# Kernel optimization log

Measured on AMD Instinct MI355X. Metric: run time of the kernel, lower is better.

Reference implementation:

```python
import jax, jax.numpy as jnp
import numpy as np
import math


def setup_inputs() -> dict:
    key = jax.random.key(0)
    k1, k2, k3 = jax.random.split(key, 3)
    B, L, H, E = 2, 2048, 8, 64
    queries = jax.random.normal(k1, (B, L, H, E), dtype=jnp.float32)
    keys = jax.random.normal(k2, (B, L, H, E), dtype=jnp.float32)
    values = jax.random.normal(k3, (B, L, H, E), dtype=jnp.float32)
    return {"queries": queries, "keys": keys, "values": values}


def reference(queries, keys, values):
    B, L, H, E = queries.shape
    scale = 1.0 / math.sqrt(E)
    # [B,H,L,S] attention scores
    scores = jnp.einsum('blhe,bshe->bhls', queries, keys)
    # causal mask: positions s > l masked to -inf (scale * -inf stays -inf)
    causal = jnp.triu(jnp.ones((L, L), dtype=bool), k=1)  # True above diagonal
    scores = jnp.where(causal[None, None, :, :], -jnp.inf, scores)
    attn = scale * scores
    SA = jax.nn.softmax(attn, axis=-1)  # dropout p=0.0 -> identity
    V = jnp.einsum('bhls,bshd->blhd', SA, values)
    return (V, SA)
```

## Files before the change

### kernel.cpp

```cpp
#include <hip/hip_runtime.h>
#include <math.h>

#define L_DIM 2048
#define H_DIM 8
#define ROWSTRIDE 512
#define NT 512
#define QSCALE 0.18033688011112042f
#define FLT_BIG 3.402823466e+38f

typedef __attribute__((ext_vector_type(8))) short short8;
typedef __attribute__((ext_vector_type(4))) float floatx4;

__device__ __forceinline__ float fexp2(float x) {
#if __has_builtin(__builtin_amdgcn_exp2f)
    return __builtin_amdgcn_exp2f(x);
#else
    return exp2f(x);
#endif
}

__device__ __forceinline__ float flog2(float x) {
#if __has_builtin(__builtin_amdgcn_logf)
    return __builtin_amdgcn_logf(x);
#else
    return log2f(x);
#endif
}

__device__ __forceinline__ unsigned int cvtpk(float lo, float hi) {
    unsigned int r;
    asm("v_cvt_pk_bf16_f32 %0, %1, %2" : "=v"(r) : "v"(lo), "v"(hi));
    return r;
}

__device__ __forceinline__ short8 pack8(float4 a, float4 b) {
    union { unsigned int u[4]; short8 v; } pk;
    pk.u[0] = cvtpk(a.x, a.y); pk.u[1] = cvtpk(a.z, a.w);
    pk.u[2] = cvtpk(b.x, b.y); pk.u[3] = cvtpk(b.z, b.w);
    return pk.v;
}

__device__ __forceinline__ short8 pack8q(float4 a, float4 b) {
    union { unsigned int u[4]; short8 v; } pk;
    pk.u[0] = cvtpk(a.x * QSCALE, a.y * QSCALE);
    pk.u[1] = cvtpk(a.z * QSCALE, a.w * QSCALE);
    pk.u[2] = cvtpk(b.x * QSCALE, b.y * QSCALE);
    pk.u[3] = cvtpk(b.z * QSCALE, b.w * QSCALE);
    return pk.v;
}

__device__ __forceinline__ int swz(int row, int col) {
    return (row << 6) + ((((col >> 3) ^ (row & 7)) << 3) | (col & 7));
}

__global__ __launch_bounds__(NT, 4)
void attn_mfma5(const float* __restrict__ Q, const float* __restrict__ K,
                const float* __restrict__ Vv, float* __restrict__ outV,
                float* __restrict__ outSA)
{
    __shared__ __align__(16) unsigned char smem[41984];
    unsigned short* Ks = (unsigned short*)(smem);
    unsigned short* Vt = (unsigned short*)(smem + 16384);
    unsigned short* Ps = (unsigned short*)(smem + 32768);
    float* Ml = (float*)(smem + 40960);
    float* Ll = (float*)(smem + 41472);
    float* Ob = (float*)(smem);

    const int t    = threadIdx.x;
    const int lane = t & 63;
    const int w    = t >> 6;
    const int g    = w >> 2;
    const int wg   = w & 3;
    const int l15  = lane & 15;
    const int quad = lane >> 4;
    const int gc   = g << 5;

    const int bid = blockIdx.x;
    const int c   = bid & 255;
    const int hf  = bid >> 8;
    const int bh  = c & 15;
    const int p   = c >> 4;
    const int qt  = hf ? p : (31 - p);
    const int h   = bh & 7;
    const int b   = bh >> 3;
    const int q0  = qt << 6;
    const int ntiles = qt + 1;

    const float* Qb = Q  + (size_t)b * L_DIM * ROWSTRIDE + h * 64;
    const float* Kb = K  + (size_t)b * L_DIM * ROWSTRIDE + h * 64;
    const float* Vb = Vv + (size_t)b * L_DIM * ROWSTRIDE + h * 64;
    float* saBase = outSA + (size_t)(b * H_DIM + h) * L_DIM * L_DIM;

    const int sr = t >> 3, sc = (t & 7) << 3;
    const int kswz = swz(sr, sc);

    short8 aQ0, aQ1;
    {
        const float* qsrc = Qb + (size_t)(q0 + 16 * wg + l15) * ROWSTRIDE + quad * 8;
        aQ0 = pack8q(*(const float4*)(qsrc),      *(const float4*)(qsrc + 4));
        aQ1 = pack8q(*(const float4*)(qsrc + 32), *(const float4*)(qsrc + 36));
    }

    float m_r[4], l_r[4];
#pragma unroll
    for (int r = 0; r < 4; ++r) { m_r[r] = -FLT_BIG; l_r[r] = 0.f; }

    {
        const float* src = Kb + (size_t)sr * ROWSTRIDE + sc;
        *(short8*)&Ks[kswz] = pack8(*(const float4*)src, *(const float4*)(src + 4));
    }
    __syncthreads();

    for (int st = 0; st < ntiles; ++st) {
        const int cur = st & 1;
        const int stp = (st + 1 < ntiles) ? (st + 1) : st;
        const float* ksrc = Kb + (size_t)((stp << 6) + sr) * ROWSTRIDE + sc;
        float4 kf0 = *(const float4*)(ksrc);
        float4 kf1 = *(const float4*)(ksrc + 4);

        const unsigned short* Kc = Ks + (cur << 12);
        floatx4 d[2];
#pragma unroll
        for (int jj = 0; jj < 2; ++jj) {
            const int sb = gc + (jj << 4) + l15;
            short8 b0 = *(const short8*)&Kc[swz(sb, quad * 8)];
            short8 b1 = *(const short8*)&Kc[swz(sb, 32 + quad * 8)];
            floatx4 acc = {0.f, 0.f, 0.f, 0.f};
            acc = __builtin_amdgcn_mfma_f32_16x16x32_bf16(aQ0, b0, acc, 0, 0, 0);
            acc = __builtin_amdgcn_mfma_f32_16x16x32_bf16(aQ1, b1, acc, 0, 0, 0);
            d[jj] = acc;
        }
        if (st == qt) {
            const int s0 = st << 6;
#pragma unroll
            for (int r = 0; r < 4; ++r) {
                const int lrow = q0 + 16 * wg + quad * 4 + r;
                float v0 = (s0 + gc +  0 + l15 <= lrow) ? d[0][r] : -INFINITY;
                float v1 = (s0 + gc + 16 + l15 <= lrow) ? d[1][r] : -INFINITY;
                const float mnew = fmaxf(m_r[r], fmaxf(v0, v1));
                float es = fexp2(v0 - mnew) + fexp2(v1 - mnew);
                l_r[r] = l_r[r] * fexp2(m_r[r] - mnew) + es;
                m_r[r] = mnew;
            }
        } else {
#pragma unroll
            for (int r = 0; r < 4; ++r) {
                float v0 = d[0][r], v1 = d[1][r];
                const float mnew = fmaxf(m_r[r], fmaxf(v0, v1));
                float es = fexp2(v0 - mnew) + fexp2(v1 - mnew);
                l_r[r] = l_r[r] * fexp2(m_r[r] - mnew) + es;
                m_r[r] = mnew;
            }
        }
        if (st + 1 < ntiles)
            *(short8*)&Ks[((cur ^ 1) << 12) + kswz] = pack8(kf0, kf1);
        __syncthreads();
    }

#pragma unroll
    for (int r = 0; r < 4; ++r) {
#pragma unroll
        for (int mk = 1; mk < 16; mk <<= 1) {
            float mo = __shfl_xor(m_r[r], mk);
            float lo = __shfl_xor(l_r[r], mk);
            float mn = fmaxf(m_r[r], mo);
            l_r[r] = l_r[r] * fexp2(m_r[r] - mn) + lo * fexp2(mo - mn);
            m_r[r] = mn;
        }
    }

    if (l15 == 0) {
#pragma unroll
        for (int r = 0; r < 4; ++r) {
            const int row = 16 * wg + quad * 4 + r;
            Ml[g * 64 + row] = m_r[r];
            Ll[g * 64 + row] = l_r[r];
        }
    }
    {
        const float* src = Kb + (size_t)sr * ROWSTRIDE + sc;
        *(short8*)&Ks[kswz] = pack8(*(const float4*)src, *(const float4*)(src + 4));
        const float* vsrc = Vb + (size_t)sr * ROWSTRIDE + sc;
        float4 f0 = *(const float4*)(vsrc);
        float4 f1 = *(const float4*)(vsrc + 4);
        unsigned int w01 = cvtpk(f0.x, f0.y), w23 = cvtpk(f0.z, f0.w);
        unsigned int w45 = cvtpk(f1.x, f1.y), w67 = cvtpk(f1.z, f1.w);
        Vt[swz(sc + 0, sr)] = (unsigned short)w01;
        Vt[swz(sc + 1, sr)] = (unsigned short)(w01 >> 16);
        Vt[swz(sc + 2, sr)] = (unsigned short)w23;
        Vt[swz(sc + 3, sr)] = (unsigned short)(w23 >> 16);
        Vt[swz(sc + 4, sr)] = (unsigned short)w45;
        Vt[swz(sc + 5, sr)] = (unsigned short)(w45 >> 16);
        Vt[swz(sc + 6, sr)] = (unsigned short)w67;
        Vt[swz(sc + 7, sr)] = (unsigned short)(w67 >> 16);
    }
    __syncthreads();

    float c_r[4];
#pragma unroll
    for (int r = 0; r < 4; ++r) {
        const int row = 16 * wg + quad * 4 + r;
        float m0 = Ml[row], m1 = Ml[64 + row];
        float l0 = Ll[row], l1 = Ll[64 + row];
        float mf = fmaxf(m0, m1);
        float lf = l0 * fexp2(m0 - mf) + l1 * fexp2(m1 - mf);
        c_r[r] = mf + flog2(lf);
    }

    floatx4 oacc[4];
#pragma unroll
    for (int j = 0; j < 4; ++j) oacc[j] = (floatx4){0.f, 0.f, 0.f, 0.f};

    for (int st = 0; st < ntiles; ++st) {
        const int cur = st & 1;
        const int stp = (st + 1 < ntiles) ? (st + 1) : st;
        const float* ksrc = Kb + (size_t)((stp << 6) + sr) * ROWSTRIDE + sc;
        const float* vsrc = Vb + (size_t)((stp << 6) + sr) * ROWSTRIDE + sc;
        float4 kf0 = *(const float4*)(ksrc);
        float4 kf1 = *(const float4*)(ksrc + 4);
        float4 vf0 = *(const float4*)(vsrc);
        float4 vf1 = *(const float4*)(vsrc + 4);

        const unsigned short* Kc = Ks + (cur << 12);
        floatx4 d[2];
#pragma unroll
        for (int jj = 0; jj < 2; ++jj) {
            const int sb = gc + (jj << 4) + l15;
            short8 b0 = *(const short8*)&Kc[swz(sb, quad * 8)];
            short8 b1 = *(const short8*)&Kc[swz(sb, 32 + quad * 8)];
            floatx4 acc = {0.f, 0.f, 0.f, 0.f};
            acc = __builtin_amdgcn_mfma_f32_16x16x32_bf16(aQ0, b0, acc, 0, 0, 0);
            acc = __builtin_amdgcn_mfma_f32_16x16x32_bf16(aQ1, b1, acc, 0, 0, 0);
            d[jj] = acc;
        }
        const int s0 = st << 6;
        if (st == qt) {
#pragma unroll
            for (int r = 0; r < 4; ++r) {
                const int lrow = q0 + 16 * wg + quad * 4 + r;
                float* sap = saBase + (size_t)lrow * L_DIM + s0 + gc + l15;
                const float cr = c_r[r];
                float p0 = (s0 + gc +      l15 <= lrow) ? fexp2(d[0][r] - cr) : 0.0f;
                float p1 = (s0 + gc + 16 + l15 <= lrow) ? fexp2(d[1][r] - cr) : 0.0f;
                sap[0] = p0; sap[16] = p1;
                unsigned int pw = cvtpk(p0, p1);
                const int prow = 16 * wg + quad * 4 + r;
                Ps[swz(prow, gc + l15)]      = (unsigned short)pw;
                Ps[swz(prow, gc + 16 + l15)] = (unsigned short)(pw >> 16);
            }
        } else {
#pragma unroll
            for (int r = 0; r < 4; ++r) {
                const int lrow = q0 + 16 * wg + quad * 4 + r;
                float* sap = saBase + (size_t)lrow * L_DIM + s0 + gc + l15;
                const float cr = c_r[r];
                float p0 = fexp2(d[0][r] - cr);
                float p1 = fexp2(d[1][r] - cr);
                sap[0] = p0; sap[16] = p1;
                unsigned int pw = cvtpk(p0, p1);
                const int prow = 16 * wg + quad * 4 + r;
                Ps[swz(prow, gc + l15)]      = (unsigned short)pw;
                Ps[swz(prow, gc + 16 + l15)] = (unsigned short)(pw >> 16);
            }
        }
        short8 aP = *(const short8*)&Ps[swz(16 * wg + l15, gc + quad * 8)];
        const unsigned short* Vc = Vt + (cur << 12);
#pragma unroll
        for (int j = 0; j < 4; ++j) {
            short8 bv = *(const short8*)&Vc[swz(16 * j + l15, gc + quad * 8)];
            oacc[j] = __builtin_amdgcn_mfma_f32_16x16x32_bf16(aP, bv, oacc[j], 0, 0, 0);
        }
        if (st + 1 < ntiles) {
            const int nb = (cur ^ 1) << 12;
            *(short8*)&Ks[nb + kswz] = pack8(kf0, kf1);
            unsigned short* Vn = Vt + nb;
            unsigned int w01 = cvtpk(vf0.x, vf0.y), w23 = cvtpk(vf0.z, vf0.w);
            unsigned int w45 = cvtpk(vf1.x, vf1.y), w67 = cvtpk(vf1.z, vf1.w);
            Vn[swz(sc + 0, sr)] = (unsigned short)w01;
            Vn[swz(sc + 1, sr)] = (unsigned short)(w01 >> 16);
            Vn[swz(sc + 2, sr)] = (unsigned short)w23;
            Vn[swz(sc + 3, sr)] = (unsigned short)(w23 >> 16);
            Vn[swz(sc + 4, sr)] = (unsigned short)w45;
            Vn[swz(sc + 5, sr)] = (unsigned short)(w45 >> 16);
            Vn[swz(sc + 6, sr)] = (unsigned short)w67;
            Vn[swz(sc + 7, sr)] = (unsigned short)(w67 >> 16);
        }
        __syncthreads();
    }

    if (g == 1) {
#pragma unroll
        for (int r = 0; r < 4; ++r) {
            const int row = 16 * wg + quad * 4 + r;
#pragma unroll
            for (int j = 0; j < 4; ++j)
                Ob[row * 65 + 16 * j + l15] = oacc[j][r];
        }
    }
    __syncthreads();
    if (g == 0) {
#pragma unroll
        for (int r = 0; r < 4; ++r) {
            const int row = 16 * wg + quad * 4 + r;
            float* op = outV + ((size_t)b * L_DIM + q0 + row) * ROWSTRIDE + h * 64 + l15;
#pragma unroll
            for (int j = 0; j < 4; ++j)
                op[16 * j] = oacc[j][r] + Ob[row * 65 + 16 * j + l15];
        }
    }

    {
        const int z0 = ntiles << 6;
        const int zr = t >> 3;
        float* rowp = saBase + (size_t)(q0 + zr) * L_DIM;
        const float4 zf = {0.f, 0.f, 0.f, 0.f};
        for (int s = z0 + (t & 7) * 4; s < L_DIM; s += 32)
            *(float4*)(rowp + s) = zf;
    }
}

extern "C" void kernel_launch(void* const* d_in, const int* in_sizes, int n_in,
                              void* d_out, int out_size, void* d_ws, size_t ws_size,
                              hipStream_t stream) {
    const float* Q  = (const float*)d_in[0];
    const float* K  = (const float*)d_in[1];
    const float* Vv = (const float*)d_in[2];
    float* out   = (float*)d_out;
    float* outV  = out;
    float* outSA = out + (size_t)2 * L_DIM * H_DIM * 64;

    dim3 grid(512);
    dim3 block(NT);
    attn_mfma5<<<grid, block, 0, stream>>>(Q, K, Vv, outV, outSA);
}
```

Measured before the change: 330.5 us.

## Process two key tiles per barrier with quad-buffered K/V and vectorized stores

Both attention passes now handle two 64-key tiles per synchronization phase, using four shared-memory buffers instead of two, which halves the number of __syncthreads and lets twice as many global loads be in flight. K rows are permuted when staged so each lane owns two adjacent score columns. That allows float2 stores to the softmax output and 32-bit packed writes to the P tile. V transposition writes packed pairs of rows as 32-bit words instead of 16-bit scalar stores. Shared memory rises from about 41 KB to 73 KB per block, which may cut occupancy below the 4 blocks requested by launch bounds.

```diff
diff --git a/kernel.cpp b/kernel.cpp
--- a/kernel.cpp
+++ b/kernel.cpp
@@ -54,16 +54,16 @@
 }
 
 __global__ __launch_bounds__(NT, 4)
-void attn_mfma5(const float* __restrict__ Q, const float* __restrict__ K,
+void attn_mfma6(const float* __restrict__ Q, const float* __restrict__ K,
                 const float* __restrict__ Vv, float* __restrict__ outV,
                 float* __restrict__ outSA)
 {
-    __shared__ __align__(16) unsigned char smem[41984];
+    __shared__ __align__(16) unsigned char smem[74752];
     unsigned short* Ks = (unsigned short*)(smem);
-    unsigned short* Vt = (unsigned short*)(smem + 16384);
-    unsigned short* Ps = (unsigned short*)(smem + 32768);
-    float* Ml = (float*)(smem + 40960);
-    float* Ll = (float*)(smem + 41472);
+    unsigned short* Vt = (unsigned short*)(smem + 32768);
+    unsigned short* Ps = (unsigned short*)(smem + 65536);
+    float* Ml = (float*)(smem + 73728);
+    float* Ll = (float*)(smem + 74240);
     float* Ob = (float*)(smem);
 
     const int t    = threadIdx.x;
@@ -85,6 +85,7 @@
     const int b   = bh >> 3;
     const int q0  = qt << 6;
     const int ntiles = qt + 1;
+    const int nphase = (ntiles + 1) >> 1;
 
     const float* Qb = Q  + (size_t)b * L_DIM * ROWSTRIDE + h * 64;
     const float* Kb = K  + (size_t)b * L_DIM * ROWSTRIDE + h * 64;
@@ -92,7 +93,26 @@
     float* saBase = outSA + (size_t)(b * H_DIM + h) * L_DIM * L_DIM;
 
     const int sr = t >> 3, sc = (t & 7) << 3;
-    const int kswz = swz(sr, sc);
+    const int kq = sr & 31;
+    const int kpr = (sr & 32) | ((kq & 1) << 4) | (kq >> 1);
+    const int kswz = swz(kpr, sc);
+
+    const int rp = t >> 4, ec = (t & 15) << 2;
+    const int vswz0 = swz(ec + 0, 2 * rp);
+    const int vswz1 = swz(ec + 1, 2 * rp);
+    const int vswz2 = swz(ec + 2, 2 * rp);
+    const int vswz3 = swz(ec + 3, 2 * rp);
+
+    auto stageK = [&](int bufi, float4 f0, float4 f1) {
+        *(short8*)&Ks[(bufi << 12) + kswz] = pack8(f0, f1);
+    };
+    auto stageV = [&](int bufi, float4 a, float4 bb) {
+        unsigned short* Vn = Vt + (bufi << 12);
+        *(unsigned int*)&Vn[vswz0] = cvtpk(a.x, bb.x);
+        *(unsigned int*)&Vn[vswz1] = cvtpk(a.y, bb.y);
+        *(unsigned int*)&Vn[vswz2] = cvtpk(a.z, bb.z);
+        *(unsigned int*)&Vn[vswz3] = cvtpk(a.w, bb.w);
+    };
 
     short8 aQ0, aQ1;
     {
@@ -105,38 +125,32 @@
 #pragma unroll
     for (int r = 0; r < 4; ++r) { m_r[r] = -FLT_BIG; l_r[r] = 0.f; }
 
-    {
-        const float* src = Kb + (size_t)sr * ROWSTRIDE + sc;
-        *(short8*)&Ks[kswz] = pack8(*(const float4*)src, *(const float4*)(src + 4));
-    }
-    __syncthreads();
-
-    for (int st = 0; st < ntiles; ++st) {
-        const int cur = st & 1;
-        const int stp = (st + 1 < ntiles) ? (st + 1) : st;
-        const float* ksrc = Kb + (size_t)((stp << 6) + sr) * ROWSTRIDE + sc;
-        float4 kf0 = *(const float4*)(ksrc);
-        float4 kf1 = *(const float4*)(ksrc + 4);
-
-        const unsigned short* Kc = Ks + (cur << 12);
-        floatx4 d[2];
-#pragma unroll
-        for (int jj = 0; jj < 2; ++jj) {
-            const int sb = gc + (jj << 4) + l15;
-            short8 b0 = *(const short8*)&Kc[swz(sb, quad * 8)];
-            short8 b1 = *(const short8*)&Kc[swz(sb, 32 + quad * 8)];
+    auto compute1 = [&](int bufi, int st) {
+        const unsigned short* Kc = Ks + (bufi << 12);
+        floatx4 d0, d1;
+        {
+            short8 b0 = *(const short8*)&Kc[swz(gc + l15, quad * 8)];
+            short8 b1 = *(const short8*)&Kc[swz(gc + l15, 32 + quad * 8)];
             floatx4 acc = {0.f, 0.f, 0.f, 0.f};
             acc = __builtin_amdgcn_mfma_f32_16x16x32_bf16(aQ0, b0, acc, 0, 0, 0);
             acc = __builtin_amdgcn_mfma_f32_16x16x32_bf16(aQ1, b1, acc, 0, 0, 0);
-            d[jj] = acc;
+            d0 = acc;
+        }
+        {
+            short8 b0 = *(const short8*)&Kc[swz(gc + 16 + l15, quad * 8)];
+            short8 b1 = *(const short8*)&Kc[swz(gc + 16 + l15, 32 + quad * 8)];
+            floatx4 acc = {0.f, 0.f, 0.f, 0.f};
+            acc = __builtin_amdgcn_mfma_f32_16x16x32_bf16(aQ0, b0, acc, 0, 0, 0);
+            acc = __builtin_amdgcn_mfma_f32_16x16x32_bf16(aQ1, b1, acc, 0, 0, 0);
+            d1 = acc;
         }
         if (st == qt) {
-            const int s0 = st << 6;
+            const int scol = (st << 6) + gc + 2 * l15;
 #pragma unroll
             for (int r = 0; r < 4; ++r) {
                 const int lrow = q0 + 16 * wg + quad * 4 + r;
-                float v0 = (s0 + gc +  0 + l15 <= lrow) ? d[0][r] : -INFINITY;
-                float v1 = (s0 + gc + 16 + l15 <= lrow) ? d[1][r] : -INFINITY;
+                float v0 = (scol     <= lrow) ? d0[r] : -INFINITY;
+                float v1 = (scol + 1 <= lrow) ? d1[r] : -INFINITY;
                 const float mnew = fmaxf(m_r[r], fmaxf(v0, v1));
                 float es = fexp2(v0 - mnew) + fexp2(v1 - mnew);
                 l_r[r] = l_r[r] * fexp2(m_r[r] - mnew) + es;
@@ -145,15 +159,39 @@
         } else {
 #pragma unroll
             for (int r = 0; r < 4; ++r) {
-                float v0 = d[0][r], v1 = d[1][r];
+                float v0 = d0[r], v1 = d1[r];
                 const float mnew = fmaxf(m_r[r], fmaxf(v0, v1));
                 float es = fexp2(v0 - mnew) + fexp2(v1 - mnew);
                 l_r[r] = l_r[r] * fexp2(m_r[r] - mnew) + es;
                 m_r[r] = mnew;
             }
         }
-        if (st + 1 < ntiles)
-            *(short8*)&Ks[((cur ^ 1) << 12) + kswz] = pack8(kf0, kf1);
+    };
+
+    {
+        const int t1 = (ntiles > 1) ? 1 : 0;
+        const float* k0 = Kb + (size_t)sr * ROWSTRIDE + sc;
+        const float* k1 = Kb + (size_t)((t1 << 6) + sr) * ROWSTRIDE + sc;
+        stageK(0, *(const float4*)k0, *(const float4*)(k0 + 4));
+        stageK(1, *(const float4*)k1, *(const float4*)(k1 + 4));
+    }
+    __syncthreads();
+
+    for (int ph = 0; ph < nphase; ++ph) {
+        const int base = ph << 1;
+        const int pb   = (ph & 1) << 1;
+        const int t2 = (base + 2 < ntiles) ? base + 2 : ntiles - 1;
+        const int t3 = (base + 3 < ntiles) ? base + 3 : ntiles - 1;
+        const float* k2 = Kb + (size_t)((t2 << 6) + sr) * ROWSTRIDE + sc;
+        const float* k3 = Kb + (size_t)((t3 << 6) + sr) * ROWSTRIDE + sc;
+        float4 a2 = *(const float4*)k2, b2 = *(const float4*)(k2 + 4);
+        float4 a3 = *(const float4*)k3, b3 = *(const float4*)(k3 + 4);
+
+        compute1(pb, base);
+        if (base + 1 < ntiles) compute1(pb + 1, base + 1);
+
+        if (base + 2 < ntiles) stageK(pb ^ 2, a2, b2);
+        if (base + 3 < ntiles) stageK((pb ^ 2) + 1, a3, b3);
         __syncthreads();
     }
 
@@ -178,21 +216,15 @@
         }
     }
     {
-        const float* src = Kb + (size_t)sr * ROWSTRIDE + sc;
-        *(short8*)&Ks[kswz] = pack8(*(const float4*)src, *(const float4*)(src + 4));
-        const float* vsrc = Vb + (size_t)sr * ROWSTRIDE + sc;
-        float4 f0 = *(const float4*)(vsrc);
-        float4 f1 = *(const float4*)(vsrc + 4);
-        unsigned int w01 = cvtpk(f0.x, f0.y), w23 = cvtpk(f0.z, f0.w);
-        unsigned int w45 = cvtpk(f1.x, f1.y), w67 = cvtpk(f1.z, f1.w);
-        Vt[swz(sc + 0, sr)] = (unsigned short)w01;
-        Vt[swz(sc + 1, sr)] = (unsigned short)(w01 >> 16);
-        Vt[swz(sc + 2, sr)] = (unsigned short)w23;
-        Vt[swz(sc + 3, sr)] = (unsigned short)(w23 >> 16);
-        Vt[swz(sc + 4, sr)] = (unsigned short)w45;
-        Vt[swz(sc + 5, sr)] = (unsigned short)(w45 >> 16);
-        Vt[swz(sc + 6, sr)] = (unsigned short)w67;
-        Vt[swz(sc + 7, sr)] = (unsigned short)(w67 >> 16);
+        const int t1 = (ntiles > 1) ? 1 : 0;
+        const float* k0 = Kb + (size_t)sr * ROWSTRIDE + sc;
+        const float* k1 = Kb + (size_t)((t1 << 6) + sr) * ROWSTRIDE + sc;
+        stageK(0, *(const float4*)k0, *(const float4*)(k0 + 4));
+        stageK(1, *(const float4*)k1, *(const float4*)(k1 + 4));
+        const float* v0p = Vb + (size_t)(2 * rp) * ROWSTRIDE + ec;
+        const float* v1p = Vb + (size_t)((t1 << 6) + 2 * rp) * ROWSTRIDE + ec;
+        stageV(0, *(const float4*)v0p, *(const float4*)(v0p + ROWSTRIDE));
+        stageV(1, *(const float4*)v1p, *(const float4*)(v1p + ROWSTRIDE));
     }
     __syncthreads();
 
@@ -211,80 +243,78 @@
 #pragma unroll
     for (int j = 0; j < 4; ++j) oacc[j] = (floatx4){0.f, 0.f, 0.f, 0.f};
 
-    for (int st = 0; st < ntiles; ++st) {
-        const int cur = st & 1;
-        const int stp = (st + 1 < ntiles) ? (st + 1) : st;
-        const float* ksrc = Kb + (size_t)((stp << 6) + sr) * ROWSTRIDE + sc;
-        const float* vsrc = Vb + (size_t)((stp << 6) + sr) * ROWSTRIDE + sc;
-        float4 kf0 = *(const float4*)(ksrc);
-        float4 kf1 = *(const float4*)(ksrc + 4);
-        float4 vf0 = *(const float4*)(vsrc);
-        float4 vf1 = *(const float4*)(vsrc + 4);
-
-        const unsigned short* Kc = Ks + (cur << 12);
-        floatx4 d[2];
-#pragma unroll
-        for (int jj = 0; jj < 2; ++jj) {
-            const int sb = gc + (jj << 4) + l15;
-            short8 b0 = *(const short8*)&Kc[swz(sb, quad * 8)];
-            short8 b1 = *(const short8*)&Kc[swz(sb, 32 + quad * 8)];
+    auto compute2 = [&](int bufi, int st) {
+        const unsigned short* Kc = Ks + (bufi << 12);
+        const unsigned short* Vc = Vt + (bufi << 12);
+        floatx4 d0, d1;
+        {
+            short8 b0 = *(const short8*)&Kc[swz(gc + l15, quad * 8)];
+            short8 b1 = *(const short8*)&Kc[swz(gc + l15, 32 + quad * 8)];
             floatx4 acc = {0.f, 0.f, 0.f, 0.f};
             acc = __builtin_amdgcn_mfma_f32_16x16x32_bf16(aQ0, b0, acc, 0, 0, 0);
             acc = __builtin_amdgcn_mfma_f32_16x16x32_bf16(aQ1, b1, acc, 0, 0, 0);
-            d[jj] = acc;
+            d0 = acc;
+        }
+        {
+            short8 b0 = *(const short8*)&Kc[swz(gc + 16 + l15, quad * 8)];
+            short8 b1 = *(const short8*)&Kc[swz(gc + 16 + l15, 32 + quad * 8)];
+            floatx4 acc = {0.f, 0.f, 0.f, 0.f};
+            acc = __builtin_amdgcn_mfma_f32_16x16x32_bf16(aQ0, b0, acc, 0, 0, 0);
+            acc = __builtin_amdgcn_mfma_f32_16x16x32_bf16(aQ1, b1, acc, 0, 0, 0);
+            d1 = acc;
         }
         const int s0 = st << 6;
+        const int scol = s0 + gc + 2 * l15;
         if (st == qt) {
 #pragma unroll
             for (int r = 0; r < 4; ++r) {
                 const int lrow = q0 + 16 * wg + quad * 4 + r;
-                float* sap = saBase + (size_t)lrow * L_DIM + s0 + gc + l15;
                 const float cr = c_r[r];
-                float p0 = (s0 + gc +      l15 <= lrow) ? fexp2(d[0][r] - cr) : 0.0f;
-                float p1 = (s0 + gc + 16 + l15 <= lrow) ? fexp2(d[1][r] - cr) : 0.0f;
-                sap[0] = p0; sap[16] = p1;
-                unsigned int pw = cvtpk(p0, p1);
-                const int prow = 16 * wg + quad * 4 + r;
-                Ps[swz(prow, gc + l15)]      = (unsigned short)pw;
-                Ps[swz(prow, gc + 16 + l15)] = (unsigned short)(pw >> 16);
+                float p0 = (scol     <= lrow) ? fexp2(d0[r] - cr) : 0.0f;
+                float p1 = (scol + 1 <= lrow) ? fexp2(d1[r] - cr) : 0.0f;
+                float2 pr; pr.x = p0; pr.y = p1;
+                *(float2*)(saBase + (size_t)lrow * L_DIM + scol) = pr;
+                *(unsigned int*)&Ps[swz(16 * wg + quad * 4 + r, gc + 2 * l15)] = cvtpk(p0, p1);
             }
         } else {
 #pragma unroll
             for (int r = 0; r < 4; ++r) {
                 const int lrow = q0 + 16 * wg + quad * 4 + r;
-                float* sap = saBase + (size_t)lrow * L_DIM + s0 + gc + l15;
                 const float cr = c_r[r];
-                float p0 = fexp2(d[0][r] - cr);
-                float p1 = fexp2(d[1][r] - cr);
-                sap[0] = p0; sap[16] = p1;
-                unsigned int pw = cvtpk(p0, p1);
-                const int prow = 16 * wg + quad * 4 + r;
-                Ps[swz(prow, gc + l15)]      = (unsigned short)pw;
-                Ps[swz(prow, gc + 16 + l15)] = (unsigned short)(pw >> 16);
+                float p0 = fexp2(d0[r] - cr);
+                float p1 = fexp2(d1[r] - cr);
+                float2 pr; pr.x = p0; pr.y = p1;
+                *(float2*)(saBase + (size_t)lrow * L_DIM + scol) = pr;
+                *(unsigned int*)&Ps[swz(16 * wg + quad * 4 + r, gc + 2 * l15)] = cvtpk(p0, p1);
             }
         }
         short8 aP = *(const short8*)&Ps[swz(16 * wg + l15, gc + quad * 8)];
-        const unsigned short* Vc = Vt + (cur << 12);
 #pragma unroll
         for (int j = 0; j < 4; ++j) {
             short8 bv = *(const short8*)&Vc[swz(16 * j + l15, gc + quad * 8)];
             oacc[j] = __builtin_amdgcn_mfma_f32_16x16x32_bf16(aP, bv, oacc[j], 0, 0, 0);
         }
-        if (st + 1 < ntiles) {
-            const int nb = (cur ^ 1) << 12;
-            *(short8*)&Ks[nb + kswz] = pack8(kf0, kf1);
-            unsigned short* Vn = Vt + nb;
-            unsigned int w01 = cvtpk(vf0.x, vf0.y), w23 = cvtpk(vf0.z, vf0.w);
-            unsigned int w45 = cvtpk(vf1.x, vf1.y), w67 = cvtpk(vf1.z, vf1.w);
-            Vn[swz(sc + 0, sr)] = (unsigned short)w01;
-            Vn[swz(sc + 1, sr)] = (unsigned short)(w01 >> 16);
-            Vn[swz(sc + 2, sr)] = (unsigned short)w23;
-            Vn[swz(sc + 3, sr)] = (unsigned short)(w23 >> 16);
-            Vn[swz(sc + 4, sr)] = (unsigned short)w45;
-            Vn[swz(sc + 5, sr)] = (unsigned short)(w45 >> 16);
-            Vn[swz(sc + 6, sr)] = (unsigned short)w67;
-            Vn[swz(sc + 7, sr)] = (unsigned short)(w67 >> 16);
-        }
+    };
+
+    for (int ph = 0; ph < nphase; ++ph) {
+        const int base = ph << 1;
+        const int pb   = (ph & 1) << 1;
+        const int t2 = (base + 2 < ntiles) ? base + 2 : ntiles - 1;
+        const int t3 = (base + 3 < ntiles) ? base + 3 : ntiles - 1;
+        const float* k2 = Kb + (size_t)((t2 << 6) + sr) * ROWSTRIDE + sc;
+        const float* k3 = Kb + (size_t)((t3 << 6) + sr) * ROWSTRIDE + sc;
+        const float* v2 = Vb + (size_t)((t2 << 6) + 2 * rp) * ROWSTRIDE + ec;
+        const float* v3 = Vb + (size_t)((t3 << 6) + 2 * rp) * ROWSTRIDE + ec;
+        float4 ka2 = *(const float4*)k2, kb2 = *(const float4*)(k2 + 4);
+        float4 ka3 = *(const float4*)k3, kb3 = *(const float4*)(k3 + 4);
+        float4 va2 = *(const float4*)v2, vb2 = *(const float4*)(v2 + ROWSTRIDE);
+        float4 va3 = *(const float4*)v3, vb3 = *(const float4*)(v3 + ROWSTRIDE);
+
+        compute2(pb, base);
+        if (base + 1 < ntiles) compute2(pb + 1, base + 1);
+
+        if (base + 2 < ntiles) { stageK(pb ^ 2, ka2, kb2); stageV(pb ^ 2, va2, vb2); }
+        if (base + 3 < ntiles) { stageK((pb ^ 2) + 1, ka3, kb3); stageV((pb ^ 2) + 1, va3, vb3); }
         __syncthreads();
     }
 
@@ -331,5 +361,5 @@
 
     dim3 grid(512);
     dim3 block(NT);
-    attn_mfma5<<<grid, block, 0, stream>>>(Q, K, Vv, outV, outSA);
-}
+    attn_mfma6<<<grid, block, 0, stream>>>(Q, K, Vv, outV, outSA);
+}
```

After: 328.8 us. No clear change (-0.5%).
